# Performance work log

Hardware: AMD Instinct MI355X
Metric: run time of the kernel (lower is better)

## Reference

```python
import jax, jax.numpy as jnp
import numpy as np

B, T, E, H = 2, 2048, 2048, 16
D = E // H


def setup_inputs() -> dict:
    key = jax.random.key(0)
    ks = jax.random.split(key, 5)
    s = 0.02
    return {
        "x": jax.random.normal(ks[0], (B, T, E), jnp.float32),
        "Wq": jax.random.normal(ks[1], (E, E), jnp.float32) * s,
        "Wk": jax.random.normal(ks[2], (E, E), jnp.float32) * s,
        "Wv": jax.random.normal(ks[3], (E, E), jnp.float32) * s,
        "Wp": jax.random.normal(ks[4], (E, E), jnp.float32) * s,
        "bp": jnp.zeros((E,), jnp.float32),
    }


def reference(x, Wq, Wk, Wv, Wp, bp):
    b, t, e = x.shape
    h, d = H, E // H
    # torch Linear: y = x @ W.T (no bias for qkv)
    Q = (x @ Wq.T).reshape(b, h, t, d)  # faithful: view without transpose
    K = (x @ Wk.T).reshape(b, h, t, d)
    V = (x @ Wv.T).reshape(b, h, t, d)
    scores = jnp.einsum("bhqd,bhkd->bhqk", Q, K)
    causal = jnp.triu(jnp.ones((t, t), bool), k=1)  # True above diagonal
    scores = jnp.where(causal, -jnp.inf, scores)
    weights = jax.nn.softmax(scores / jnp.sqrt(jnp.float32(d)), axis=-1)
    # dropout p=0.0 (eval) -> identity
    ctx = jnp.einsum("bhqk,bhkd->bhqd", weights, V)  # (b,h,t,d)
    ctx = ctx.transpose(0, 2, 1, 3).reshape(b, t, e)
    return ctx @ Wp.T + bp
```

## Files before the change

### kernel.cpp

```cpp
#include <hip/hip_runtime.h>

#define SEQ   2048
#define EMB   2048
#define NHEAD 16
#define HDIM  128
#define ROWSM 4096

typedef float  f32x4   __attribute__((ext_vector_type(4)));
typedef float  f32x16  __attribute__((ext_vector_type(16)));
typedef __bf16 bf16x8  __attribute__((ext_vector_type(8)));

__device__ __forceinline__ unsigned short f2bf(float f) {
  union { __bf16 b; unsigned short u; } v; v.b = (__bf16)f; return v.u;
}
__device__ __forceinline__ unsigned int pk2(float a, float b) {
  return (unsigned int)f2bf(a) | ((unsigned int)f2bf(b) << 16);
}
__device__ __forceinline__ float max3f(float a, float b, float c) {
  return fmaxf(fmaxf(a, b), c);
}

__device__ __forceinline__ void gload16(const void* g, void* l) {
  __builtin_amdgcn_global_load_lds(
      (__attribute__((address_space(1))) const unsigned int*)g,
      (__attribute__((address_space(3))) unsigned int*)l,
      16, 0, 0);
}

__global__ void cvt_bf16(const float* __restrict__ in,
                         unsigned short* __restrict__ out, int n4) {
  int i = blockIdx.x * 256 + threadIdx.x;
  if (i >= n4) return;
  float4 v = ((const float4*)in)[i];
  ushort4 o;
  o.x = f2bf(v.x); o.y = f2bf(v.y); o.z = f2bf(v.z); o.w = f2bf(v.w);
  ((ushort4*)out)[i] = o;
}

__global__ void cvt_bf16_3(const float* __restrict__ i0, const float* __restrict__ i1,
                           const float* __restrict__ i2, unsigned short* __restrict__ o0,
                           unsigned short* __restrict__ o1, unsigned short* __restrict__ o2,
                           int n4) {
  const float* in = (blockIdx.z == 0) ? i0 : (blockIdx.z == 1) ? i1 : i2;
  unsigned short* out = (blockIdx.z == 0) ? o0 : (blockIdx.z == 1) ? o1 : o2;
  int i = blockIdx.x * 256 + threadIdx.x;
  if (i >= n4) return;
  float4 v = ((const float4*)in)[i];
  ushort4 o;
  o.x = f2bf(v.x); o.y = f2bf(v.y); o.z = f2bf(v.z); o.w = f2bf(v.w);
  ((ushort4*)out)[i] = o;
}

template <int STORE_F32>
__global__ __launch_bounds__(512, 1) void gemm8(
    const unsigned short* __restrict__ A,
    const unsigned short* __restrict__ B0, const unsigned short* __restrict__ B1,
    const unsigned short* __restrict__ B2,
    void* __restrict__ Cbase, const float* __restrict__ bias) {
  __shared__ __align__(16) unsigned short At[2][128 * 64];
  __shared__ __align__(16) unsigned short Bt[2][256 * 64];
  const unsigned short* Bm = (blockIdx.z == 0) ? B0 : (blockIdx.z == 1) ? B1 : B2;

  const int tid  = threadIdx.x;
  const int lane = tid & 63;
  const int w    = tid >> 6;
  const int wr   = w >> 2;
  const int wc   = w & 3;
  const int lg   = lane >> 4;
  const int lc   = lane & 15;

  const int bid = blockIdx.x;
  const int xcd = bid & 7;
  const int j   = bid >> 3;
  const int mt  = xcd * 4 + (j >> 3);
  const int nt  = j & 7;
  const int m0 = mt * 128;
  const int n0 = nt * 256;

  const int srow8 = lane >> 3;
  const int sslot = (lane & 7) ^ srow8;
  const int NT = EMB / 64;

  auto stageA = [&](int ts) {
    if (ts >= NT) return;
    int buf = ts & 1, k0 = ts * 64;
#pragma unroll
    for (int rr = 0; rr < 2; ++rr) {
      int c = w + rr * 8;
      int row = c * 8 + srow8;
      gload16(A + (size_t)(m0 + row) * EMB + k0 + sslot * 8, (char*)&At[buf][0] + c * 1024);
    }
  };
  auto stageBlow = [&](int ts) {
    if (ts >= NT) return;
    int buf = ts & 1, k0 = ts * 64;
#pragma unroll
    for (int rr = 0; rr < 2; ++rr) {
      int i = w + rr * 8;
      int c = (i >> 2) * 8 + (i & 3);
      int row = c * 8 + srow8;
      gload16(Bm + (size_t)(n0 + row) * EMB + k0 + sslot * 8, (char*)&Bt[buf][0] + c * 1024);
    }
  };
  auto stageBhigh = [&](int ts) {
    if (ts >= NT) return;
    int buf = ts & 1, k0 = ts * 64;
#pragma unroll
    for (int rr = 0; rr < 2; ++rr) {
      int i = w + rr * 8;
      int c = (i >> 2) * 8 + 4 + (i & 3);
      int row = c * 8 + srow8;
      gload16(Bm + (size_t)(n0 + row) * EMB + k0 + sslot * 8, (char*)&Bt[buf][0] + c * 1024);
    }
  };

  f32x4 acc[4][4] = {};
  bf16x8 afr[4][2], bfr0[2][2], bfr1[2][2];

  stageA(0); stageBlow(0); stageBhigh(0); stageA(1); stageBlow(1);
  asm volatile("s_waitcnt vmcnt(6)" ::: "memory");
  __builtin_amdgcn_s_barrier();

  for (int t = 0; t < NT; ++t) {
    const char* ab = (const char*)&At[t & 1][0];
    const char* bb = (const char*)&Bt[t & 1][0];

#pragma unroll
    for (int ni = 0; ni < 2; ++ni)
#pragma unroll
      for (int kk = 0; kk < 2; ++kk) {
        int row = wc * 64 + ni * 16 + lc;
        bfr0[ni][kk] = *(const bf16x8*)(bb + row * 128 + ((((kk << 2) | lg) ^ (lc & 7)) << 4));
      }
#pragma unroll
    for (int mi = 0; mi < 4; ++mi)
#pragma unroll
      for (int kk = 0; kk < 2; ++kk) {
        int row = wr * 64 + mi * 16 + lc;
        afr[mi][kk] = *(const bf16x8*)(ab + row * 128 + ((((kk << 2) | lg) ^ (lc & 7)) << 4));
      }
    stageBhigh(t + 1);
    __builtin_amdgcn_s_barrier();
    asm volatile("s_waitcnt lgkmcnt(0)" ::: "memory");
    __builtin_amdgcn_sched_barrier(0);
    __builtin_amdgcn_s_setprio(1);
#pragma unroll
    for (int mi = 0; mi < 4; ++mi)
#pragma unroll
      for (int ni = 0; ni < 2; ++ni)
#pragma unroll
        for (int kk = 0; kk < 2; ++kk)
          acc[mi][ni] = __builtin_amdgcn_mfma_f32_16x16x32_bf16(
              afr[mi][kk], bfr0[ni][kk], acc[mi][ni], 0, 0, 0);
    __builtin_amdgcn_s_setprio(0);
    if (t + 1 < NT) asm volatile("s_waitcnt vmcnt(6)" ::: "memory");
    else            asm volatile("s_waitcnt vmcnt(0)" ::: "memory");
    __builtin_amdgcn_s_barrier();

#pragma unroll
    for (int ni = 0; ni < 2; ++ni)
#pragma unroll
      for (int kk = 0; kk < 2; ++kk) {
        int row = wc * 64 + 32 + ni * 16 + lc;
        bfr1[ni][kk] = *(const bf16x8*)(bb + row * 128 + ((((kk << 2) | lg) ^ (lc & 7)) << 4));
      }
    stageA(t + 2); stageBlow(t + 2);
    __builtin_amdgcn_s_barrier();
    asm volatile("s_waitcnt lgkmcnt(0)" ::: "memory");
    __builtin_amdgcn_sched_barrier(0);
    __builtin_amdgcn_s_setprio(1);
#pragma unroll
    for (int mi = 0; mi < 4; ++mi)
#pragma unroll
      for (int ni = 0; ni < 2; ++ni)
#pragma unroll
        for (int kk = 0; kk < 2; ++kk)
          acc[mi][2 + ni] = __builtin_amdgcn_mfma_f32_16x16x32_bf16(
              afr[mi][kk], bfr1[ni][kk], acc[mi][2 + ni], 0, 0, 0);
    __builtin_amdgcn_s_setprio(0);
    if (t + 2 < NT)      asm volatile("s_waitcnt vmcnt(6)" ::: "memory");
    else if (t + 1 < NT) asm volatile("s_waitcnt vmcnt(2)" ::: "memory");
    __builtin_amdgcn_s_barrier();
  }

#pragma unroll
  for (int mi = 0; mi < 4; ++mi)
#pragma unroll
    for (int ni = 0; ni < 4; ++ni) {
      int col = n0 + wc * 64 + ((ni >> 1) * 32) + (ni & 1) * 16 + lc;
#pragma unroll
      for (int rr = 0; rr < 4; ++rr) {
        int row = m0 + wr * 64 + mi * 16 + lg * 4 + rr;
        if (STORE_F32) {
          ((float*)Cbase)[(size_t)row * EMB + col] = acc[mi][ni][rr] + bias[col];
        } else {
          ((unsigned short*)Cbase + (size_t)blockIdx.z * ROWSM * EMB)
              [(size_t)row * EMB + col] = f2bf(acc[mi][ni][rr]);
        }
      }
    }
}

__global__ __launch_bounds__(256, 2) void attn_causal(
    const unsigned short* __restrict__ Pq, const unsigned short* __restrict__ Pk,
    const unsigned short* __restrict__ Pv, unsigned short* __restrict__ ctx) {
  __shared__ __align__(16) unsigned short Ks[128 * 128];
  __shared__ __align__(16) unsigned short Vt[128 * 128];

  const int tid  = threadIdx.x;
  const int lane = tid & 63;
  const int w    = tid >> 6;
  const int ql   = lane & 31;
  const int hi   = lane >> 5;
  const int lg   = lane >> 4;
  const int lc   = lane & 15;

  const int bid = blockIdx.x;
  const int xcd = bid & 7;
  const int jj_ = bid >> 3;
  const int hh  = jj_ >> 4;
  const int bh  = xcd * 4 + hh;
  const int b   = bh >> 4;
  const int h   = bh & 15;
  const int qtr = jj_ & 15;
  const int qt  = (hh >= 2) ? (15 - qtr) : qtr;
  const int q0 = qt * 128;
  const int qw = q0 + w * 32;
  const int qg = qw + ql;

  const size_t hoff = (size_t)bh * SEQ * HDIM;
  const unsigned short* Q  = Pq + hoff;
  const unsigned short* Kh = Pk + hoff;
  const unsigned short* Vh = Pv + hoff;

  bf16x8 bq[8];
#pragma unroll
  for (int d8 = 0; d8 < 8; ++d8)
    bq[d8] = *(const bf16x8*)(Q + (size_t)qg * HDIM + d8 * 16 + hi * 8);

  const float NEG = -3.0e38f;
  f32x16 o[4];
#pragma unroll
  for (int dt = 0; dt < 4; ++dt)
#pragma unroll
    for (int r = 0; r < 16; ++r) o[dt][r] = 0.f;
  float m_r = NEG, l_r = 0.f;

  const float Cs   = 0.12753123161692858f;
  const float TDEF = 62.7f;

  const int nt128 = qt + 1;
  for (int tt = 0; tt < nt128; ++tt) {
    const int kv0 = tt * 128;
    if (tt) __syncthreads();
#pragma unroll
    for (int ii = 0; ii < 8; ++ii) {
      int i = w * 8 + ii;
      int r = i * 4 + lg;
      int sd = lc ^ (r & 7);
      gload16(Kh + (size_t)(kv0 + r) * HDIM + sd * 8, (char*)Ks + i * 1024);
    }
#pragma unroll 1
    for (int hv = 0; hv < 2; ++hv) {
      uint4 vr[4];
      const unsigned short* Vs = Vh + (size_t)(kv0 + hv * 64) * HDIM;
#pragma unroll
      for (int uu = 0; uu < 2; ++uu) {
        int u = tid + uu * 256;
        int kp = u >> 4, dg = u & 15;
        int k = kp * 2, d0 = dg * 8;
        vr[uu * 2]     = *(const uint4*)(Vs + (size_t)k * HDIM + d0);
        vr[uu * 2 + 1] = *(const uint4*)(Vs + (size_t)(k + 1) * HDIM + d0);
      }
#pragma unroll
      for (int uu = 0; uu < 2; ++uu) {
        int u = tid + uu * 256;
        int kp = u >> 4, dg = u & 15;
        int k = kp * 2, d0 = dg * 8;
        const unsigned short* e0 = (const unsigned short*)&vr[uu * 2];
        const unsigned short* e1 = (const unsigned short*)&vr[uu * 2 + 1];
#pragma unroll
        for (int jj = 0; jj < 8; ++jj) {
          int d = d0 + jj;
          int slot = ((hv << 3) | (k >> 3)) ^ jj ^ (dg & 7);
          int byteoff = d * 256 + (slot << 4) + (k & 7) * 2;
          *(unsigned int*)((char*)Vt + byteoff) =
              (unsigned int)e0[jj] | ((unsigned int)e1[jj] << 16);
        }
      }
    }
    __syncthreads();

#pragma unroll 1
    for (int hf = 0; hf < 2; ++hf) {
      const int kv0h = kv0 + hf * 64;
      if (kv0h > qw + 31) continue;
      const bool s1on = (kv0h + 32 <= qw + 31);
      const bool diag = (kv0h + 63 > qw);
      const char* ksb = (const char*)Ks + hf * 64 * 256;

      f32x16 c0, c1;
#pragma unroll
      for (int r = 0; r < 16; ++r) { c0[r] = 0.f; c1[r] = s1on ? 0.f : NEG; }
      __builtin_amdgcn_s_setprio(1);
#pragma unroll
      for (int d8 = 0; d8 < 8; ++d8) {
        bf16x8 ak = *(const bf16x8*)(ksb + ql * 256 +
                                     (((d8 * 2 + hi) ^ (ql & 7)) << 4));
        c0 = __builtin_amdgcn_mfma_f32_32x32x16_bf16(ak, bq[d8], c0, 0, 0, 0);
      }
      if (s1on) {
#pragma unroll
        for (int d8 = 0; d8 < 8; ++d8) {
          bf16x8 ak = *(const bf16x8*)(ksb + (32 + ql) * 256 +
                                       (((d8 * 2 + hi) ^ (ql & 7)) << 4));
          c1 = __builtin_amdgcn_mfma_f32_32x32x16_bf16(ak, bq[d8], c1, 0, 0, 0);
        }
      }
      __builtin_amdgcn_s_setprio(0);

      if (diag) {
#pragma unroll
        for (int r = 0; r < 16; ++r) {
          int kvl = (r & 3) + 8 * (r >> 2) + 4 * hi;
          if (kv0h + kvl > qg) c0[r] = NEG;
          if (s1on && kv0h + 32 + kvl > qg) c1[r] = NEG;
        }
      }
      float rm;
      {
        float a0 = max3f(c0[0],  c0[1],  c0[2]);
        float a1 = max3f(c0[3],  c0[4],  c0[5]);
        float a2 = max3f(c0[6],  c0[7],  c0[8]);
        float a3 = max3f(c0[9],  c0[10], c0[11]);
        float a4 = max3f(c0[12], c0[13], c0[14]);
        float a5 = max3f(c0[15], c1[0],  c1[1]);
        float a6 = max3f(c1[2],  c1[3],  c1[4]);
        float a7 = max3f(c1[5],  c1[6],  c1[7]);
        float a8 = max3f(c1[8],  c1[9],  c1[10]);
        float a9 = max3f(c1[11], c1[12], c1[13]);
        float aa = fmaxf(c1[14], c1[15]);
        float b0 = max3f(a0, a1, a2);
        float b1 = max3f(a3, a4, a5);
        float b2 = max3f(a6, a7, a8);
        float b3 = max3f(a9, aa, NEG);
        rm = fmaxf(fmaxf(b0, b1), fmaxf(b2, b3));
      }
      rm = fmaxf(rm, __shfl_xor(rm, 32));

      if (__any(rm > m_r + TDEF)) {
        float mnew = fmaxf(m_r, rm);
        float alpha = exp2f((m_r - mnew) * Cs);
        m_r = mnew;
        l_r *= alpha;
#pragma unroll
        for (int r = 0; r < 16; ++r) {
          float ar = __shfl(alpha, (r & 3) + 8 * (r >> 2) + 4 * hi);
#pragma unroll
          for (int dt = 0; dt < 4; ++dt) o[dt][r] *= ar;
        }
      }
#pragma unroll
      for (int r = 0; r < 16; ++r) {
        c0[r] = exp2f((c0[r] - m_r) * Cs);
        c1[r] = exp2f((c1[r] - m_r) * Cs);
      }
      float ps = 0.f;
#pragma unroll
      for (int r = 0; r < 16; ++r) ps += c0[r] + c1[r];
      ps += __shfl_xor(ps, 32);
      l_r += ps;

      bf16x8 pa[4];
#pragma unroll
      for (int t4 = 0; t4 < 4; ++t4) {
        const f32x16& cc = (t4 < 2) ? c0 : c1;
        const int rA = (t4 & 1) * 8;
        unsigned int pkL0 = pk2(cc[rA + 0], cc[rA + 1]);
        unsigned int pkL1 = pk2(cc[rA + 2], cc[rA + 3]);
        unsigned int pkH0 = pk2(cc[rA + 4], cc[rA + 5]);
        unsigned int pkH1 = pk2(cc[rA + 6], cc[rA + 7]);
        unsigned int give0 = hi ? pkL0 : pkH0;
        unsigned int give1 = hi ? pkL1 : pkH1;
        unsigned int keep0 = hi ? pkH0 : pkL0;
        unsigned int keep1 = hi ? pkH1 : pkL1;
        unsigned int recv0 = __shfl_xor(give0, 32);
        unsigned int recv1 = __shfl_xor(give1, 32);
        union { unsigned int u[4]; bf16x8 v; } pu;
        pu.u[0] = hi ? recv0 : keep0;
        pu.u[1] = hi ? recv1 : keep1;
        pu.u[2] = hi ? keep0 : recv0;
        pu.u[3] = hi ? keep1 : recv1;
        pa[t4] = pu.v;
      }
      __builtin_amdgcn_s_setprio(1);
#pragma unroll
      for (int t4 = 0; t4 < 4; ++t4) {
        if (diag && kv0h + t4 * 16 > qw + 31) continue;
#pragma unroll
        for (int dt = 0; dt < 4; ++dt) {
          int d = dt * 32 + ql;
          int slot = ((hf << 3) | (t4 << 1) | hi) ^ (d & 7) ^ ((d >> 3) & 7);
          bf16x8 bv = *(const bf16x8*)((const char*)Vt + d * 256 + (slot << 4));
          o[dt] = __builtin_amdgcn_mfma_f32_32x32x16_bf16(pa[t4], bv, o[dt], 0, 0, 0);
        }
      }
      __builtin_amdgcn_s_setprio(0);
    }
  }

  float linv = 1.0f / l_r;
  unsigned short* outp = ctx + (size_t)b * SEQ * EMB + (size_t)h * HDIM;
#pragma unroll
  for (int r = 0; r < 16; ++r) {
    int kvl = (r & 3) + 8 * (r >> 2) + 4 * hi;
    float lr = __shfl(linv, kvl);
    int qrow = qw + kvl;
#pragma unroll
    for (int dt = 0; dt < 4; ++dt)
      outp[(size_t)qrow * EMB + dt * 32 + ql] = f2bf(o[dt][r] * lr);
  }
}

extern "C" void kernel_launch(void* const* d_in, const int* in_sizes, int n_in,
                              void* d_out, int out_size, void* d_ws, size_t ws_size,
                              hipStream_t stream) {
  const float* x  = (const float*)d_in[0];
  const float* Wq = (const float*)d_in[1];
  const float* Wk = (const float*)d_in[2];
  const float* Wv = (const float*)d_in[3];
  const float* Wp = (const float*)d_in[4];
  const float* bp = (const float*)d_in[5];

  char* ws = (char*)d_ws;
  unsigned short* xb = (unsigned short*)ws;
  unsigned short* Wb = (unsigned short*)(ws + (size_t)(16u << 20));
  unsigned short* Pq = (unsigned short*)(ws + (size_t)(24u << 20));
  unsigned short* Pk = (unsigned short*)(ws + (size_t)(40u << 20));
  unsigned short* Pv = (unsigned short*)(ws + (size_t)(56u << 20));
  unsigned short* WvS = (unsigned short*)d_out;
  unsigned short* WkS = (unsigned short*)d_out + (size_t)4 * 1024 * 1024;

  const int nX4 = ROWSM * EMB / 4;
  const int nW4 = EMB * EMB / 4;

  cvt_bf16<<<nX4 / 256, 256, 0, stream>>>(x, xb, nX4);
  cvt_bf16_3<<<dim3(nW4 / 256, 1, 3), 256, 0, stream>>>(Wq, Wk, Wv, Wb, WkS, WvS, nW4);

  gemm8<0><<<dim3(256, 1, 3), 512, 0, stream>>>(xb, Wb, WkS, WvS, Pq, nullptr);

  attn_causal<<<512, 256, 0, stream>>>(Pq, Pk, Pv, xb);

  cvt_bf16<<<nW4 / 256, 256, 0, stream>>>(Wp, Wb, nW4);
  gemm8<1><<<dim3(256, 1, 1), 512, 0, stream>>>(xb, Wb, Wb, Wb, d_out, bp);
}
```

Baseline: 260.9 us.

## Fuse QKV projections into one GEMM with 256x192 tiles over concatenated weights

The Q, K and V weight matrices are now converted into one contiguous bf16 buffer, so the three projections run as a single GEMM with N=6144. That GEMM uses a 256x192 block tile with 512 blocks, and the epilogue routes each column to the Pq, Pk or Pv output. The larger M tile raises arithmetic intensity, and the single launch of 512 blocks fills the device better than the earlier 3x256 grid of 128x256 tiles. In exchange the kernel holds more accumulators per thread and uses more LDS, which may hurt register allocation or scheduling.

```diff
diff --git a/kernel.cpp b/kernel.cpp
--- a/kernel.cpp
+++ b/kernel.cpp
@@ -38,28 +38,23 @@
 }
 
 __global__ void cvt_bf16_3(const float* __restrict__ i0, const float* __restrict__ i1,
-                           const float* __restrict__ i2, unsigned short* __restrict__ o0,
-                           unsigned short* __restrict__ o1, unsigned short* __restrict__ o2,
+                           const float* __restrict__ i2, unsigned short* __restrict__ o,
                            int n4) {
   const float* in = (blockIdx.z == 0) ? i0 : (blockIdx.z == 1) ? i1 : i2;
-  unsigned short* out = (blockIdx.z == 0) ? o0 : (blockIdx.z == 1) ? o1 : o2;
+  unsigned short* out = o + (size_t)blockIdx.z * EMB * EMB;
   int i = blockIdx.x * 256 + threadIdx.x;
   if (i >= n4) return;
   float4 v = ((const float4*)in)[i];
-  ushort4 o;
-  o.x = f2bf(v.x); o.y = f2bf(v.y); o.z = f2bf(v.z); o.w = f2bf(v.w);
-  ((ushort4*)out)[i] = o;
-}
-
-template <int STORE_F32>
-__global__ __launch_bounds__(512, 1) void gemm8(
-    const unsigned short* __restrict__ A,
-    const unsigned short* __restrict__ B0, const unsigned short* __restrict__ B1,
-    const unsigned short* __restrict__ B2,
-    void* __restrict__ Cbase, const float* __restrict__ bias) {
-  __shared__ __align__(16) unsigned short At[2][128 * 64];
-  __shared__ __align__(16) unsigned short Bt[2][256 * 64];
-  const unsigned short* Bm = (blockIdx.z == 0) ? B0 : (blockIdx.z == 1) ? B1 : B2;
+  ushort4 o4;
+  o4.x = f2bf(v.x); o4.y = f2bf(v.y); o4.z = f2bf(v.z); o4.w = f2bf(v.w);
+  ((ushort4*)out)[i] = o4;
+}
+
+__global__ __launch_bounds__(512, 1) void gemm192_qkv(
+    const unsigned short* __restrict__ A, const unsigned short* __restrict__ B,
+    unsigned short* __restrict__ Cb) {
+  __shared__ __align__(16) unsigned short At[2][256 * 64];
+  __shared__ __align__(16) unsigned short Bt[2][192 * 64];
 
   const int tid  = threadIdx.x;
   const int lane = tid & 63;
@@ -72,6 +67,142 @@
   const int bid = blockIdx.x;
   const int xcd = bid & 7;
   const int j   = bid >> 3;
+  const int mt  = xcd * 2 + (j >> 5);
+  const int nt  = j & 31;
+  const int m0 = mt * 256;
+  const int n0 = nt * 192;
+
+  const int srow8 = lane >> 3;
+  const int sslot = (lane & 7) ^ srow8;
+  const int NT = EMB / 64;
+
+  auto stageAeven = [&](int ts) {
+    if (ts >= NT) return;
+    int buf = ts & 1, k0 = ts * 64;
+    { int c = w;      int row = c * 8 + srow8;
+      gload16(A + (size_t)(m0 + row) * EMB + k0 + sslot * 8, (char*)&At[buf][0] + c * 1024); }
+    { int c = 16 + w; int row = c * 8 + srow8;
+      gload16(A + (size_t)(m0 + row) * EMB + k0 + sslot * 8, (char*)&At[buf][0] + c * 1024); }
+  };
+  auto stageAodd = [&](int ts) {
+    if (ts >= NT) return;
+    int buf = ts & 1, k0 = ts * 64;
+    { int c = 8 + w;  int row = c * 8 + srow8;
+      gload16(A + (size_t)(m0 + row) * EMB + k0 + sslot * 8, (char*)&At[buf][0] + c * 1024); }
+    { int c = 24 + w; int row = c * 8 + srow8;
+      gload16(A + (size_t)(m0 + row) * EMB + k0 + sslot * 8, (char*)&At[buf][0] + c * 1024); }
+  };
+  auto stageB = [&](int ts) {
+    if (ts >= NT) return;
+    int buf = ts & 1, k0 = ts * 64;
+#pragma unroll
+    for (int s = 0; s < 3; ++s) {
+      int c = w + s * 8;
+      int row = c * 8 + srow8;
+      gload16(B + (size_t)(n0 + row) * EMB + k0 + sslot * 8, (char*)&Bt[buf][0] + c * 1024);
+    }
+  };
+
+  f32x4 acc[8][3] = {};
+  bf16x8 afr[4][2], bfr[3][2];
+
+  stageAeven(0); stageB(0); stageAodd(0); stageAeven(1); stageB(1);
+  asm volatile("s_waitcnt vmcnt(7)" ::: "memory");
+  __builtin_amdgcn_s_barrier();
+
+  for (int t = 0; t < NT; ++t) {
+    const char* ab = (const char*)&At[t & 1][0];
+    const char* bb = (const char*)&Bt[t & 1][0];
+
+#pragma unroll
+    for (int ni = 0; ni < 3; ++ni)
+#pragma unroll
+      for (int kk = 0; kk < 2; ++kk) {
+        int row = wc * 48 + ni * 16 + lc;
+        bfr[ni][kk] = *(const bf16x8*)(bb + row * 128 + ((((kk << 2) | lg) ^ (lc & 7)) << 4));
+      }
+#pragma unroll
+    for (int mi = 0; mi < 4; ++mi)
+#pragma unroll
+      for (int kk = 0; kk < 2; ++kk) {
+        int row = wr * 128 + mi * 16 + lc;
+        afr[mi][kk] = *(const bf16x8*)(ab + row * 128 + ((((kk << 2) | lg) ^ (lc & 7)) << 4));
+      }
+    stageAodd(t + 1);
+    __builtin_amdgcn_s_barrier();
+    asm volatile("s_waitcnt lgkmcnt(0)" ::: "memory");
+    __builtin_amdgcn_sched_barrier(0);
+    __builtin_amdgcn_s_setprio(1);
+#pragma unroll
+    for (int mi = 0; mi < 4; ++mi)
+#pragma unroll
+      for (int ni = 0; ni < 3; ++ni)
+#pragma unroll
+        for (int kk = 0; kk < 2; ++kk)
+          acc[mi][ni] = __builtin_amdgcn_mfma_f32_16x16x32_bf16(
+              afr[mi][kk], bfr[ni][kk], acc[mi][ni], 0, 0, 0);
+    __builtin_amdgcn_s_setprio(0);
+    if (t + 1 < NT) asm volatile("s_waitcnt vmcnt(7)" ::: "memory");
+    else            asm volatile("s_waitcnt vmcnt(0)" ::: "memory");
+    __builtin_amdgcn_s_barrier();
+
+#pragma unroll
+    for (int mi = 0; mi < 4; ++mi)
+#pragma unroll
+      for (int kk = 0; kk < 2; ++kk) {
+        int row = wr * 128 + 64 + mi * 16 + lc;
+        afr[mi][kk] = *(const bf16x8*)(ab + row * 128 + ((((kk << 2) | lg) ^ (lc & 7)) << 4));
+      }
+    stageAeven(t + 2); stageB(t + 2);
+    __builtin_amdgcn_s_barrier();
+    asm volatile("s_waitcnt lgkmcnt(0)" ::: "memory");
+    __builtin_amdgcn_sched_barrier(0);
+    __builtin_amdgcn_s_setprio(1);
+#pragma unroll
+    for (int mi = 0; mi < 4; ++mi)
+#pragma unroll
+      for (int ni = 0; ni < 3; ++ni)
+#pragma unroll
+        for (int kk = 0; kk < 2; ++kk)
+          acc[4 + mi][ni] = __builtin_amdgcn_mfma_f32_16x16x32_bf16(
+              afr[mi][kk], bfr[ni][kk], acc[4 + mi][ni], 0, 0, 0);
+    __builtin_amdgcn_s_setprio(0);
+    if (t + 2 < NT)      asm volatile("s_waitcnt vmcnt(7)" ::: "memory");
+    else if (t + 1 < NT) asm volatile("s_waitcnt vmcnt(2)" ::: "memory");
+    __builtin_amdgcn_s_barrier();
+  }
+
+#pragma unroll
+  for (int mi = 0; mi < 8; ++mi)
+#pragma unroll
+    for (int ni = 0; ni < 3; ++ni) {
+      int col = n0 + wc * 48 + ni * 16 + lc;
+      unsigned short* dst = Cb + (size_t)(col >> 11) * ROWSM * EMB + (col & 2047);
+#pragma unroll
+      for (int rr = 0; rr < 4; ++rr) {
+        int row = m0 + wr * 128 + mi * 16 + lg * 4 + rr;
+        dst[(size_t)row * EMB] = f2bf(acc[mi][ni][rr]);
+      }
+    }
+}
+
+__global__ __launch_bounds__(512, 1) void gemm_p8(
+    const unsigned short* __restrict__ A, const unsigned short* __restrict__ B,
+    float* __restrict__ Cout, const float* __restrict__ bias) {
+  __shared__ __align__(16) unsigned short At[2][128 * 64];
+  __shared__ __align__(16) unsigned short Bt[2][256 * 64];
+
+  const int tid  = threadIdx.x;
+  const int lane = tid & 63;
+  const int w    = tid >> 6;
+  const int wr   = w >> 2;
+  const int wc   = w & 3;
+  const int lg   = lane >> 4;
+  const int lc   = lane & 15;
+
+  const int bid = blockIdx.x;
+  const int xcd = bid & 7;
+  const int j   = bid >> 3;
   const int mt  = xcd * 4 + (j >> 3);
   const int nt  = j & 7;
   const int m0 = mt * 128;
@@ -99,7 +230,7 @@
       int i = w + rr * 8;
       int c = (i >> 2) * 8 + (i & 3);
       int row = c * 8 + srow8;
-      gload16(Bm + (size_t)(n0 + row) * EMB + k0 + sslot * 8, (char*)&Bt[buf][0] + c * 1024);
+      gload16(B + (size_t)(n0 + row) * EMB + k0 + sslot * 8, (char*)&Bt[buf][0] + c * 1024);
     }
   };
   auto stageBhigh = [&](int ts) {
@@ -110,7 +241,7 @@
       int i = w + rr * 8;
       int c = (i >> 2) * 8 + 4 + (i & 3);
       int row = c * 8 + srow8;
-      gload16(Bm + (size_t)(n0 + row) * EMB + k0 + sslot * 8, (char*)&Bt[buf][0] + c * 1024);
+      gload16(B + (size_t)(n0 + row) * EMB + k0 + sslot * 8, (char*)&Bt[buf][0] + c * 1024);
     }
   };
 
@@ -191,12 +322,7 @@
 #pragma unroll
       for (int rr = 0; rr < 4; ++rr) {
         int row = m0 + wr * 64 + mi * 16 + lg * 4 + rr;
-        if (STORE_F32) {
-          ((float*)Cbase)[(size_t)row * EMB + col] = acc[mi][ni][rr] + bias[col];
-        } else {
-          ((unsigned short*)Cbase + (size_t)blockIdx.z * ROWSM * EMB)
-              [(size_t)row * EMB + col] = f2bf(acc[mi][ni][rr]);
-        }
+        Cout[(size_t)row * EMB + col] = acc[mi][ni][rr] + bias[col];
       }
     }
 }
@@ -438,19 +564,18 @@
   unsigned short* Pq = (unsigned short*)(ws + (size_t)(24u << 20));
   unsigned short* Pk = (unsigned short*)(ws + (size_t)(40u << 20));
   unsigned short* Pv = (unsigned short*)(ws + (size_t)(56u << 20));
-  unsigned short* WvS = (unsigned short*)d_out;
-  unsigned short* WkS = (unsigned short*)d_out + (size_t)4 * 1024 * 1024;
+  unsigned short* WB3 = (unsigned short*)d_out;
 
   const int nX4 = ROWSM * EMB / 4;
   const int nW4 = EMB * EMB / 4;
 
   cvt_bf16<<<nX4 / 256, 256, 0, stream>>>(x, xb, nX4);
-  cvt_bf16_3<<<dim3(nW4 / 256, 1, 3), 256, 0, stream>>>(Wq, Wk, Wv, Wb, WkS, WvS, nW4);
-
-  gemm8<0><<<dim3(256, 1, 3), 512, 0, stream>>>(xb, Wb, WkS, WvS, Pq, nullptr);
+  cvt_bf16_3<<<dim3(nW4 / 256, 1, 3), 256, 0, stream>>>(Wq, Wk, Wv, WB3, nW4);
+
+  gemm192_qkv<<<512, 512, 0, stream>>>(xb, WB3, Pq);
 
   attn_causal<<<512, 256, 0, stream>>>(Pq, Pk, Pv, xb);
 
   cvt_bf16<<<nW4 / 256, 256, 0, stream>>>(Wp, Wb, nW4);
-  gemm8<1><<<dim3(256, 1, 1), 512, 0, stream>>>(xb, Wb, Wb, Wb, d_out, bp);
-}
+  gemm_p8<<<256, 512, 0, stream>>>(xb, Wb, (float*)d_out, bp);
+}
```

Measured after the change: 256.9 us. Within noise of the previous version (-1.6%).
